# Kernel tuning notes

Hardware: AMD Instinct MI355X
Metric: run time of the kernel (lower is better)

## Reference

```python
import jax, jax.numpy as jnp
import numpy as np

N_NODES = 50000
N_EDGES = 500000
IN_DIM = 64
OUT_DIM = 64
NUM_RELS = 16


def setup_inputs() -> dict:
    key = jax.random.key(0)
    ks = jax.random.split(key, 8)
    h = jax.random.normal(ks[0], (N_NODES, IN_DIM), dtype=jnp.float32)
    he = jax.random.normal(ks[1], (N_EDGES, IN_DIM), dtype=jnp.float32)
    src = jax.random.randint(ks[2], (N_EDGES,), 0, N_NODES)
    dst = jax.random.randint(ks[3], (N_EDGES,), 0, N_NODES)
    rel = jax.random.randint(ks[4], (N_EDGES,), 0, NUM_RELS)
    # xavier-ish scales
    W_shared = jax.random.normal(ks[5], (OUT_DIM, IN_DIM), dtype=jnp.float32) * (2.0 / (IN_DIM + OUT_DIM)) ** 0.5
    W_attn = jax.random.normal(ks[6], (1, 3 * OUT_DIM), dtype=jnp.float32) * (2.0 / (3 * OUT_DIM + 1)) ** 0.5
    W_rel = jax.random.normal(ks[7], (NUM_RELS, IN_DIM, OUT_DIM), dtype=jnp.float32) * (2.0 / (IN_DIM + OUT_DIM)) ** 0.5
    return {"h": h, "he": he, "src": src, "dst": dst, "rel": rel,
            "W_shared": W_shared, "W_attn": W_attn, "W_rel": W_rel}


def reference(h, he, src, dst, rel, W_shared, W_attn, W_rel):
    # --- edge attention: a = attn_fc([z_src, z_edge, z_dst]) (raw linear score, no softmax in original) ---
    Z = h @ W_shared.T                      # [N, out] project all nodes once
    ze = he @ W_shared.T                    # [E, out]
    # split attn weight to avoid materializing [E, 3*out] concat
    Wa_s, Wa_e, Wa_d = jnp.split(W_attn, 3, axis=1)   # each [1, out]
    a = Z[src] @ Wa_s.T + ze @ Wa_e.T + Z[dst] @ Wa_d.T   # [E, 1]
    # --- message: msg = (h_src @ W_rel[rel]) * a ---
    # compute per-(node, relation) transform once [N, R, out], then gather per edge
    H_all = jnp.einsum('ni,rio->nro', h, W_rel)          # [N, R, out]
    msg = H_all[src, rel] * a                             # [E, out]
    # --- scatter-sum aggregation into destination nodes ---
    out = jax.ops.segment_sum(msg, dst, num_segments=N_NODES)  # [N, out]
    # apply_func: activation (relu), no bias
    return jax.nn.relu(out)
```

## Files before the change

kernel.cpp:

```cpp
#include <hip/hip_runtime.h>
#include <math.h>

#define N_NODES 50000
#define N_EDGES 500000
#define NUM_RELS 16
#define G3 64

typedef _Float16 f16x8 __attribute__((ext_vector_type(8)));
typedef float    f32x4 __attribute__((ext_vector_type(4)));


__global__ void kz(int* counts, int* cursor) {
    if (threadIdx.x < NUM_RELS) { counts[threadIdx.x] = 0; cursor[threadIdx.x] = 0; }
}

__global__ __launch_bounds__(256) void k_node(
    const float* __restrict__ h,
    const float* __restrict__ W_shared, const float* __restrict__ W_attn,
    const int* __restrict__ rel,
    float* __restrict__ sn, float* __restrict__ dn,
    float4* __restrict__ out4, int* __restrict__ counts) {
    __shared__ float sus[64], sud[64];
    __shared__ int hist[NUM_RELS];
    const int t = threadIdx.x, bid = blockIdx.x, nb = gridDim.x;
    if (t < 64) {
        float us = 0.f, ud = 0.f;
        for (int o = 0; o < 64; ++o) {
            float w = W_shared[o * 64 + t];
            us = fmaf(w, W_attn[o],       us);
            ud = fmaf(w, W_attn[128 + o], ud);
        }
        sus[t] = us; sud[t] = ud;
    }
    if (t < NUM_RELS) hist[t] = 0;
    __syncthreads();

    int n = bid * 256 + t;
    if (n < N_NODES) {
        const float* hp = h + (size_t)n * 64;
        float s = 0.f, d = 0.f;
#pragma unroll
        for (int i = 0; i < 64; i += 4) {
            float4 v = *(const float4*)(hp + i);
            s = fmaf(v.x, sus[i], s);     s = fmaf(v.y, sus[i + 1], s);
            s = fmaf(v.z, sus[i + 2], s); s = fmaf(v.w, sus[i + 3], s);
            d = fmaf(v.x, sud[i], d);     d = fmaf(v.y, sud[i + 1], d);
            d = fmaf(v.z, sud[i + 2], d); d = fmaf(v.w, sud[i + 3], d);
        }
        sn[n] = s; dn[n] = d;
        float4 z = make_float4(0.f, 0.f, 0.f, 0.f);
#pragma unroll
        for (int i = 0; i < 16; ++i) out4[(size_t)n * 16 + i] = z;
    }
    for (int e = bid * 256 + t; e < N_EDGES; e += nb * 256)
        atomicAdd(&hist[rel[e]], 1);
    __syncthreads();
    if (t < NUM_RELS && hist[t]) atomicAdd(&counts[t], hist[t]);
}

__global__ __launch_bounds__(256) void k_ae(
    const float4* __restrict__ he4,
    const int* __restrict__ src, const int* __restrict__ dst,
    const int* __restrict__ rel,
    const float* __restrict__ W_shared, const float* __restrict__ W_attn,
    const float* __restrict__ sn, const float* __restrict__ dn,
    const int* __restrict__ counts, int* __restrict__ cursor,
    int* __restrict__ srcs, int* __restrict__ dsts, float* __restrict__ aes) {
    __shared__ float sve[64];
    __shared__ int hist[NUM_RELS], bbase[NUM_RELS], soffs[NUM_RELS];
    const int t = threadIdx.x, bid = blockIdx.x, nb = gridDim.x;
    if (t < 64) {
        float ve = 0.f;
        for (int o = 0; o < 64; ++o)
            ve = fmaf(W_shared[o * 64 + t], W_attn[64 + o], ve);
        sve[t] = ve;
    }
    if (t == 0) {
        int acc = 0;
        for (int j = 0; j < NUM_RELS; ++j) { soffs[j] = acc; acc += counts[j]; }
    }
    for (int e0 = bid * 256; e0 < N_EDGES; e0 += nb * 256) {
        __syncthreads();
        if (t < NUM_RELS) hist[t] = 0;
        __syncthreads();
        int e = e0 + t;
        bool valid = (e < N_EDGES);
        int r = 0, lpos = 0, s_ = 0, d_ = 0; float aev = 0.f;
        if (valid) {
            s_ = src[e]; d_ = dst[e]; r = rel[e];
            const float4* hr = he4 + (size_t)e * 16;
            float acc = 0.f;
#pragma unroll
            for (int i = 0; i < 16; ++i) {
                float4 v = hr[i];
                float4 u = *(const float4*)(sve + 4 * i);
                acc += v.x * u.x + v.y * u.y + v.z * u.z + v.w * u.w;
            }
            aev = acc + sn[s_] + dn[d_];
            lpos = atomicAdd(&hist[r], 1);
        }
        __syncthreads();
        if (t < NUM_RELS) bbase[t] = hist[t] ? atomicAdd(&cursor[t], hist[t]) : 0;
        __syncthreads();
        if (valid) {
            int p = soffs[r] + bbase[r] + lpos;
            srcs[p] = s_; dsts[p] = d_; aes[p] = aev;
        }
    }
}

__global__ __launch_bounds__(256, 4) void k_mfma(
    const float* __restrict__ h, const float* __restrict__ W_rel,
    const int* __restrict__ counts,
    const int* __restrict__ srcs, const int* __restrict__ dsts,
    const float* __restrict__ aes, float* __restrict__ out)
{
    const int t = threadIdx.x;
    const int lane = t & 63;
    const int quad = lane >> 4;
    const int col  = lane & 15;
    const int wib  = t >> 6;
    const int r    = blockIdx.x & 15;
    const int g    = blockIdx.x >> 4;
    const int wr   = g * 4 + wib;
    const int WPR  = G3 * 4;

    int begin = 0, cr = 0;
#pragma unroll
    for (int j = 0; j < NUM_RELS; ++j) {
        int c = counts[j];
        if (j < r) begin += c;
        if (j == r) cr = c;
    }
    begin = __builtin_amdgcn_readfirstlane(begin);
    const int end = __builtin_amdgcn_readfirstlane(begin + cr);

    const float* Wb = W_rel + (size_t)r * 4096;

    for (int half = 0; half < 2; ++half) {
        f16x8 bh[2][2], bl[2][2];
#pragma unroll
        for (int kb = 0; kb < 2; ++kb)
#pragma unroll
            for (int n2 = 0; n2 < 2; ++n2)
#pragma unroll
                for (int j = 0; j < 8; ++j) {
                    float w = Wb[(kb * 32 + quad * 8 + j) * 64 + (half * 2 + n2) * 16 + col];
                    _Float16 hi = (_Float16)w;
                    bh[kb][n2][j] = hi;
                    bl[kb][n2][j] = (_Float16)(w - (float)hi);
                }

        for (int base = begin + wr * 16; base < end; base += WPR * 16) {
            int m16 = end - base; if (m16 > 16) m16 = 16;
            const int ridx = base + (col < m16 ? col : m16 - 1);
            const int   sv = srcs[ridx];
            const int   dv = dsts[ridx];
            const float av = (col < m16) ? aes[ridx] : 0.f;

            f16x8 ah[2], al[2];
            const float* hp = h + (size_t)sv * 64 + quad * 8;
#pragma unroll
            for (int kb = 0; kb < 2; ++kb) {
                float4 x = *(const float4*)(hp + kb * 32);
                float4 y = *(const float4*)(hp + kb * 32 + 4);
                float xs[8] = {x.x, x.y, x.z, x.w, y.x, y.y, y.z, y.w};
#pragma unroll
                for (int j = 0; j < 8; ++j) {
                    _Float16 hi = (_Float16)xs[j];
                    ah[kb][j] = hi;
                    al[kb][j] = (_Float16)(xs[j] - (float)hi);
                }
            }

            f32x4 acc0 = {0.f, 0.f, 0.f, 0.f};
            f32x4 acc1 = {0.f, 0.f, 0.f, 0.f};
#pragma unroll
            for (int kb = 0; kb < 2; ++kb) {
                acc0 = __builtin_amdgcn_mfma_f32_16x16x32_f16(ah[kb], bh[kb][0], acc0, 0, 0, 0);
                acc0 = __builtin_amdgcn_mfma_f32_16x16x32_f16(ah[kb], bl[kb][0], acc0, 0, 0, 0);
                acc0 = __builtin_amdgcn_mfma_f32_16x16x32_f16(al[kb], bh[kb][0], acc0, 0, 0, 0);
                acc1 = __builtin_amdgcn_mfma_f32_16x16x32_f16(ah[kb], bh[kb][1], acc1, 0, 0, 0);
                acc1 = __builtin_amdgcn_mfma_f32_16x16x32_f16(ah[kb], bl[kb][1], acc1, 0, 0, 0);
                acc1 = __builtin_amdgcn_mfma_f32_16x16x32_f16(al[kb], bh[kb][1], acc1, 0, 0, 0);
            }

#pragma unroll
            for (int reg = 0; reg < 4; ++reg) {
                const int m = quad * 4 + reg;
                const int   dm = __shfl(dv, m, 64);
                const float am = __shfl(av, m, 64);
                float* op = out + (size_t)dm * 64 + half * 32 + col;
                unsafeAtomicAdd(op,      am * acc0[reg]);
                unsafeAtomicAdd(op + 16, am * acc1[reg]);
            }
        }
    }
}

__global__ __launch_bounds__(256) void k_relu(float4* __restrict__ out4) {
    for (int i = blockIdx.x * 256 + threadIdx.x; i < N_NODES * 16; i += gridDim.x * 256) {
        float4 v = out4[i];
        v.x = fmaxf(v.x, 0.f); v.y = fmaxf(v.y, 0.f);
        v.z = fmaxf(v.z, 0.f); v.w = fmaxf(v.w, 0.f);
        out4[i] = v;
    }
}

extern "C" void kernel_launch(void* const* d_in, const int* in_sizes, int n_in,
                              void* d_out, int out_size, void* d_ws, size_t ws_size,
                              hipStream_t stream) {
    const float*  h        = (const float*)d_in[0];
    const float4* he4      = (const float4*)d_in[1];
    const int*    src      = (const int*)d_in[2];
    const int*    dst      = (const int*)d_in[3];
    const int*    rel      = (const int*)d_in[4];
    const float*  W_shared = (const float*)d_in[5];
    const float*  W_attn   = (const float*)d_in[6];
    const float*  W_rel    = (const float*)d_in[7];
    float*        out      = (float*)d_out;

    int*   counts = (int*)d_ws + 192;
    int*   cursor = (int*)d_ws + 228;
    float* sn     = (float*)d_ws + 256;
    float* dn     = (float*)d_ws + 50256;
    int*   srcs   = (int*)d_ws + 100352;
    int*   dsts   = (int*)d_ws + 600352;
    float* aes    = (float*)d_ws + 1100352;

    kz<<<1, 64, 0, stream>>>(counts, cursor);
    k_node<<<(N_NODES + 255) / 256, 256, 0, stream>>>(h, W_shared, W_attn, rel,
                                                      sn, dn, (float4*)out, counts);
    k_ae<<<1024, 256, 0, stream>>>(he4, src, dst, rel, W_shared, W_attn,
                                   sn, dn, counts, cursor, srcs, dsts, aes);
    k_mfma<<<NUM_RELS * G3, 256, 0, stream>>>(h, W_rel, counts, srcs, dsts, aes, out);
    k_relu<<<1024, 256, 0, stream>>>((float4*)out);
}
```

Measured before the change: 350.9 us.

## Precompute fp16 hi/lo split of h, split halves across blocks, prefetch gathers

```diff
diff --git a/kernel.cpp b/kernel.cpp
--- a/kernel.cpp
+++ b/kernel.cpp
@@ -4,9 +4,10 @@
 #define N_NODES 50000
 #define N_EDGES 500000
 #define NUM_RELS 16
-#define G3 64
+#define GH 64
 
 typedef _Float16 f16x8 __attribute__((ext_vector_type(8)));
+typedef _Float16 f16x4 __attribute__((ext_vector_type(4)));
 typedef float    f32x4 __attribute__((ext_vector_type(4)));
 
 
@@ -19,7 +20,8 @@
     const float* __restrict__ W_shared, const float* __restrict__ W_attn,
     const int* __restrict__ rel,
     float* __restrict__ sn, float* __restrict__ dn,
-    float4* __restrict__ out4, int* __restrict__ counts) {
+    float4* __restrict__ out4, int* __restrict__ counts,
+    _Float16* __restrict__ h_hi, _Float16* __restrict__ h_lo) {
     __shared__ float sus[64], sud[64];
     __shared__ int hist[NUM_RELS];
     const int t = threadIdx.x, bid = blockIdx.x, nb = gridDim.x;
@@ -46,6 +48,13 @@
             s = fmaf(v.z, sus[i + 2], s); s = fmaf(v.w, sus[i + 3], s);
             d = fmaf(v.x, sud[i], d);     d = fmaf(v.y, sud[i + 1], d);
             d = fmaf(v.z, sud[i + 2], d); d = fmaf(v.w, sud[i + 3], d);
+            f16x4 hi, lo;
+            hi[0] = (_Float16)v.x; lo[0] = (_Float16)(v.x - (float)hi[0]);
+            hi[1] = (_Float16)v.y; lo[1] = (_Float16)(v.y - (float)hi[1]);
+            hi[2] = (_Float16)v.z; lo[2] = (_Float16)(v.z - (float)hi[2]);
+            hi[3] = (_Float16)v.w; lo[3] = (_Float16)(v.w - (float)hi[3]);
+            *(f16x4*)(h_hi + (size_t)n * 64 + i) = hi;
+            *(f16x4*)(h_lo + (size_t)n * 64 + i) = lo;
         }
         sn[n] = s; dn[n] = d;
         float4 z = make_float4(0.f, 0.f, 0.f, 0.f);
@@ -110,7 +119,8 @@
 }
 
 __global__ __launch_bounds__(256, 4) void k_mfma(
-    const float* __restrict__ h, const float* __restrict__ W_rel,
+    const _Float16* __restrict__ h_hi, const _Float16* __restrict__ h_lo,
+    const float* __restrict__ W_rel,
     const int* __restrict__ counts,
     const int* __restrict__ srcs, const int* __restrict__ dsts,
     const float* __restrict__ aes, float* __restrict__ out)
@@ -120,10 +130,13 @@
     const int quad = lane >> 4;
     const int col  = lane & 15;
     const int wib  = t >> 6;
-    const int r    = blockIdx.x & 15;
-    const int g    = blockIdx.x >> 4;
+    const int rh   = blockIdx.x & 31;
+    const int r    = rh & 15;
+    const int half = rh >> 4;
+    const int g    = blockIdx.x >> 5;
     const int wr   = g * 4 + wib;
-    const int WPR  = G3 * 4;
+    const int WPR  = GH * 4;
+    const int STEP = WPR * 16;
 
     int begin = 0, cr = 0;
 #pragma unroll
@@ -136,65 +149,79 @@
     const int end = __builtin_amdgcn_readfirstlane(begin + cr);
 
     const float* Wb = W_rel + (size_t)r * 4096;
-
-    for (int half = 0; half < 2; ++half) {
-        f16x8 bh[2][2], bl[2][2];
-#pragma unroll
-        for (int kb = 0; kb < 2; ++kb)
-#pragma unroll
-            for (int n2 = 0; n2 < 2; ++n2)
-#pragma unroll
-                for (int j = 0; j < 8; ++j) {
-                    float w = Wb[(kb * 32 + quad * 8 + j) * 64 + (half * 2 + n2) * 16 + col];
-                    _Float16 hi = (_Float16)w;
-                    bh[kb][n2][j] = hi;
-                    bl[kb][n2][j] = (_Float16)(w - (float)hi);
-                }
-
-        for (int base = begin + wr * 16; base < end; base += WPR * 16) {
-            int m16 = end - base; if (m16 > 16) m16 = 16;
-            const int ridx = base + (col < m16 ? col : m16 - 1);
-            const int   sv = srcs[ridx];
-            const int   dv = dsts[ridx];
-            const float av = (col < m16) ? aes[ridx] : 0.f;
-
-            f16x8 ah[2], al[2];
-            const float* hp = h + (size_t)sv * 64 + quad * 8;
-#pragma unroll
-            for (int kb = 0; kb < 2; ++kb) {
-                float4 x = *(const float4*)(hp + kb * 32);
-                float4 y = *(const float4*)(hp + kb * 32 + 4);
-                float xs[8] = {x.x, x.y, x.z, x.w, y.x, y.y, y.z, y.w};
-#pragma unroll
-                for (int j = 0; j < 8; ++j) {
-                    _Float16 hi = (_Float16)xs[j];
-                    ah[kb][j] = hi;
-                    al[kb][j] = (_Float16)(xs[j] - (float)hi);
-                }
+    f16x8 bh[2][2], bl[2][2];
+#pragma unroll
+    for (int kb = 0; kb < 2; ++kb)
+#pragma unroll
+        for (int n2 = 0; n2 < 2; ++n2)
+#pragma unroll
+            for (int j = 0; j < 8; ++j) {
+                float w = Wb[(kb * 32 + quad * 8 + j) * 64 + (half * 2 + n2) * 16 + col];
+                _Float16 hi = (_Float16)w;
+                bh[kb][n2][j] = hi;
+                bl[kb][n2][j] = (_Float16)(w - (float)hi);
             }
 
-            f32x4 acc0 = {0.f, 0.f, 0.f, 0.f};
-            f32x4 acc1 = {0.f, 0.f, 0.f, 0.f};
-#pragma unroll
-            for (int kb = 0; kb < 2; ++kb) {
-                acc0 = __builtin_amdgcn_mfma_f32_16x16x32_f16(ah[kb], bh[kb][0], acc0, 0, 0, 0);
-                acc0 = __builtin_amdgcn_mfma_f32_16x16x32_f16(ah[kb], bl[kb][0], acc0, 0, 0, 0);
-                acc0 = __builtin_amdgcn_mfma_f32_16x16x32_f16(al[kb], bh[kb][0], acc0, 0, 0, 0);
-                acc1 = __builtin_amdgcn_mfma_f32_16x16x32_f16(ah[kb], bh[kb][1], acc1, 0, 0, 0);
-                acc1 = __builtin_amdgcn_mfma_f32_16x16x32_f16(ah[kb], bl[kb][1], acc1, 0, 0, 0);
-                acc1 = __builtin_amdgcn_mfma_f32_16x16x32_f16(al[kb], bh[kb][1], acc1, 0, 0, 0);
-            }
-
-#pragma unroll
-            for (int reg = 0; reg < 4; ++reg) {
-                const int m = quad * 4 + reg;
-                const int   dm = __shfl(dv, m, 64);
-                const float am = __shfl(av, m, 64);
-                float* op = out + (size_t)dm * 64 + half * 32 + col;
-                unsafeAtomicAdd(op,      am * acc0[reg]);
-                unsafeAtomicAdd(op + 16, am * acc1[reg]);
-            }
-        }
+    int base = begin + wr * 16;
+    if (base >= end) return;
+
+    int sv0, dv0; float av0;
+    {
+        int m16 = end - base; if (m16 > 16) m16 = 16;
+        int ridx = base + (col < m16 ? col : m16 - 1);
+        sv0 = srcs[ridx]; dv0 = dsts[ridx];
+        av0 = (col < m16) ? aes[ridx] : 0.f;
+    }
+    f16x8 ah0, ah1, al0, al1;
+    {
+        const _Float16* ph = h_hi + (size_t)sv0 * 64 + quad * 8;
+        const _Float16* pl = h_lo + (size_t)sv0 * 64 + quad * 8;
+        ah0 = *(const f16x8*)ph;        ah1 = *(const f16x8*)(ph + 32);
+        al0 = *(const f16x8*)pl;        al1 = *(const f16x8*)(pl + 32);
+    }
+
+    for (; base < end; base += STEP) {
+        const int nb = base + STEP;
+        int sv1 = 0, dv1 = 0; float av1 = 0.f;
+        f16x8 nah0, nah1, nal0, nal1;
+        if (nb < end) {
+            int m16 = end - nb; if (m16 > 16) m16 = 16;
+            int ridx = nb + (col < m16 ? col : m16 - 1);
+            sv1 = srcs[ridx]; dv1 = dsts[ridx];
+            av1 = (col < m16) ? aes[ridx] : 0.f;
+            const _Float16* ph = h_hi + (size_t)sv1 * 64 + quad * 8;
+            const _Float16* pl = h_lo + (size_t)sv1 * 64 + quad * 8;
+            nah0 = *(const f16x8*)ph;   nah1 = *(const f16x8*)(ph + 32);
+            nal0 = *(const f16x8*)pl;   nal1 = *(const f16x8*)(pl + 32);
+        }
+
+        f32x4 acc0 = {0.f, 0.f, 0.f, 0.f};
+        f32x4 acc1 = {0.f, 0.f, 0.f, 0.f};
+        acc0 = __builtin_amdgcn_mfma_f32_16x16x32_f16(ah0, bh[0][0], acc0, 0, 0, 0);
+        acc1 = __builtin_amdgcn_mfma_f32_16x16x32_f16(ah0, bh[0][1], acc1, 0, 0, 0);
+        acc0 = __builtin_amdgcn_mfma_f32_16x16x32_f16(ah0, bl[0][0], acc0, 0, 0, 0);
+        acc1 = __builtin_amdgcn_mfma_f32_16x16x32_f16(ah0, bl[0][1], acc1, 0, 0, 0);
+        acc0 = __builtin_amdgcn_mfma_f32_16x16x32_f16(al0, bh[0][0], acc0, 0, 0, 0);
+        acc1 = __builtin_amdgcn_mfma_f32_16x16x32_f16(al0, bh[0][1], acc1, 0, 0, 0);
+        acc0 = __builtin_amdgcn_mfma_f32_16x16x32_f16(ah1, bh[1][0], acc0, 0, 0, 0);
+        acc1 = __builtin_amdgcn_mfma_f32_16x16x32_f16(ah1, bh[1][1], acc1, 0, 0, 0);
+        acc0 = __builtin_amdgcn_mfma_f32_16x16x32_f16(ah1, bl[1][0], acc0, 0, 0, 0);
+        acc1 = __builtin_amdgcn_mfma_f32_16x16x32_f16(ah1, bl[1][1], acc1, 0, 0, 0);
+        acc0 = __builtin_amdgcn_mfma_f32_16x16x32_f16(al1, bh[1][0], acc0, 0, 0, 0);
+        acc1 = __builtin_amdgcn_mfma_f32_16x16x32_f16(al1, bh[1][1], acc1, 0, 0, 0);
+
+#pragma unroll
+        for (int reg = 0; reg < 4; ++reg) {
+            const int m = quad * 4 + reg;
+            const int   dm = __shfl(dv0, m, 64);
+            const float am = __shfl(av0, m, 64);
+            float* op = out + (size_t)dm * 64 + half * 32 + col;
+            unsafeAtomicAdd(op,      am * acc0[reg]);
+            unsafeAtomicAdd(op + 16, am * acc1[reg]);
+        }
+
+        sv0 = sv1; dv0 = dv1; av0 = av1;
+        ah0 = nah0; ah1 = nah1; al0 = nal0; al1 = nal1;
     }
 }
 
@@ -220,19 +247,22 @@
     const float*  W_rel    = (const float*)d_in[7];
     float*        out      = (float*)d_out;
 
-    int*   counts = (int*)d_ws + 192;
-    int*   cursor = (int*)d_ws + 228;
-    float* sn     = (float*)d_ws + 256;
-    float* dn     = (float*)d_ws + 50256;
-    int*   srcs   = (int*)d_ws + 100352;
-    int*   dsts   = (int*)d_ws + 600352;
-    float* aes    = (float*)d_ws + 1100352;
+    int*      counts = (int*)d_ws + 192;
+    int*      cursor = (int*)d_ws + 228;
+    float*    sn     = (float*)d_ws + 256;
+    float*    dn     = (float*)d_ws + 50256;
+    int*      srcs   = (int*)d_ws + 100352;
+    int*      dsts   = (int*)d_ws + 600352;
+    float*    aes    = (float*)d_ws + 1100352;
+    _Float16* h_hi   = (_Float16*)((int*)d_ws + 1600352);
+    _Float16* h_lo   = (_Float16*)((int*)d_ws + 3200352);
 
     kz<<<1, 64, 0, stream>>>(counts, cursor);
     k_node<<<(N_NODES + 255) / 256, 256, 0, stream>>>(h, W_shared, W_attn, rel,
-                                                      sn, dn, (float4*)out, counts);
-    k_ae<<<1024, 256, 0, stream>>>(he4, src, dst, rel, W_shared, W_attn,
+                                                      sn, dn, (float4*)out, counts,
+                                                      h_hi, h_lo);
+    k_ae<<<2048, 256, 0, stream>>>(he4, src, dst, rel, W_shared, W_attn,
                                    sn, dn, counts, cursor, srcs, dsts, aes);
-    k_mfma<<<NUM_RELS * G3, 256, 0, stream>>>(h, W_rel, counts, srcs, dsts, aes, out);
+    k_mfma<<<32 * GH, 256, 0, stream>>>(h_hi, h_lo, W_rel, counts, srcs, dsts, aes, out);
     k_relu<<<1024, 256, 0, stream>>>((float4*)out);
 }
```

After: 358.6 us. +2.2%, slower.

## Bucket edges by destination block and relation, aggregate in shared memory

Applied to the files above, without the earlier changes.

```diff
diff --git a/kernel.cpp b/kernel.cpp
--- a/kernel.cpp
+++ b/kernel.cpp
@@ -4,24 +4,28 @@
 #define N_NODES 50000
 #define N_EDGES 500000
 #define NUM_RELS 16
-#define G3 64
+#define DSTB 64
+#define NBLK_AGG 782
+#define NKEY (NBLK_AGG * NUM_RELS)
 
 typedef _Float16 f16x8 __attribute__((ext_vector_type(8)));
+typedef _Float16 f16x4 __attribute__((ext_vector_type(4)));
 typedef float    f32x4 __attribute__((ext_vector_type(4)));
 
 
-__global__ void kz(int* counts, int* cursor) {
-    if (threadIdx.x < NUM_RELS) { counts[threadIdx.x] = 0; cursor[threadIdx.x] = 0; }
+__global__ void kz(int* __restrict__ counts, int* __restrict__ cursor) {
+    int i = blockIdx.x * 256 + threadIdx.x;
+    if (i < NKEY) { counts[i] = 0; cursor[i] = 0; }
 }
 
 __global__ __launch_bounds__(256) void k_node(
     const float* __restrict__ h,
     const float* __restrict__ W_shared, const float* __restrict__ W_attn,
-    const int* __restrict__ rel,
+    const int* __restrict__ dst, const int* __restrict__ rel,
     float* __restrict__ sn, float* __restrict__ dn,
-    float4* __restrict__ out4, int* __restrict__ counts) {
+    int* __restrict__ counts,
+    _Float16* __restrict__ h_hi, _Float16* __restrict__ h_lo) {
     __shared__ float sus[64], sud[64];
-    __shared__ int hist[NUM_RELS];
     const int t = threadIdx.x, bid = blockIdx.x, nb = gridDim.x;
     if (t < 64) {
         float us = 0.f, ud = 0.f;
@@ -32,7 +36,6 @@
         }
         sus[t] = us; sud[t] = ud;
     }
-    if (t < NUM_RELS) hist[t] = 0;
     __syncthreads();
 
     int n = bid * 256 + t;
@@ -46,16 +49,45 @@
             s = fmaf(v.z, sus[i + 2], s); s = fmaf(v.w, sus[i + 3], s);
             d = fmaf(v.x, sud[i], d);     d = fmaf(v.y, sud[i + 1], d);
             d = fmaf(v.z, sud[i + 2], d); d = fmaf(v.w, sud[i + 3], d);
+            f16x4 hi, lo;
+            hi[0] = (_Float16)v.x; lo[0] = (_Float16)(v.x - (float)hi[0]);
+            hi[1] = (_Float16)v.y; lo[1] = (_Float16)(v.y - (float)hi[1]);
+            hi[2] = (_Float16)v.z; lo[2] = (_Float16)(v.z - (float)hi[2]);
+            hi[3] = (_Float16)v.w; lo[3] = (_Float16)(v.w - (float)hi[3]);
+            *(f16x4*)(h_hi + (size_t)n * 64 + i) = hi;
+            *(f16x4*)(h_lo + (size_t)n * 64 + i) = lo;
         }
         sn[n] = s; dn[n] = d;
-        float4 z = make_float4(0.f, 0.f, 0.f, 0.f);
-#pragma unroll
-        for (int i = 0; i < 16; ++i) out4[(size_t)n * 16 + i] = z;
-    }
-    for (int e = bid * 256 + t; e < N_EDGES; e += nb * 256)
-        atomicAdd(&hist[rel[e]], 1);
-    __syncthreads();
-    if (t < NUM_RELS && hist[t]) atomicAdd(&counts[t], hist[t]);
+    }
+    for (int e = bid * 256 + t; e < N_EDGES; e += nb * 256) {
+        int key = (dst[e] >> 6) * NUM_RELS + rel[e];
+        atomicAdd(&counts[key], 1);
+    }
+}
+
+__global__ __launch_bounds__(1024) void k_scan(const int* __restrict__ counts,
+                                               int* __restrict__ offs) {
+    __shared__ int part[1024];
+    const int t = threadIdx.x;
+    const int C = 13;
+    int s = 0;
+    for (int j = 0; j < C; ++j) {
+        int idx = t * C + j;
+        if (idx < NKEY) s += counts[idx];
+    }
+    part[t] = s;
+    __syncthreads();
+    if (t == 0) {
+        int a = 0;
+        for (int i = 0; i < 1024; ++i) { int v = part[i]; part[i] = a; a += v; }
+    }
+    __syncthreads();
+    int a = part[t];
+    for (int j = 0; j < C; ++j) {
+        int idx = t * C + j;
+        if (idx < NKEY)       { offs[idx] = a; a += counts[idx]; }
+        else if (idx == NKEY) { offs[idx] = a; }
+    }
 }
 
 __global__ __launch_bounds__(256) void k_ae(
@@ -64,10 +96,9 @@
     const int* __restrict__ rel,
     const float* __restrict__ W_shared, const float* __restrict__ W_attn,
     const float* __restrict__ sn, const float* __restrict__ dn,
-    const int* __restrict__ counts, int* __restrict__ cursor,
+    const int* __restrict__ offs, int* __restrict__ cursor,
     int* __restrict__ srcs, int* __restrict__ dsts, float* __restrict__ aes) {
     __shared__ float sve[64];
-    __shared__ int hist[NUM_RELS], bbase[NUM_RELS], soffs[NUM_RELS];
     const int t = threadIdx.x, bid = blockIdx.x, nb = gridDim.x;
     if (t < 64) {
         float ve = 0.f;
@@ -75,135 +106,112 @@
             ve = fmaf(W_shared[o * 64 + t], W_attn[64 + o], ve);
         sve[t] = ve;
     }
-    if (t == 0) {
-        int acc = 0;
-        for (int j = 0; j < NUM_RELS; ++j) { soffs[j] = acc; acc += counts[j]; }
-    }
-    for (int e0 = bid * 256; e0 < N_EDGES; e0 += nb * 256) {
-        __syncthreads();
-        if (t < NUM_RELS) hist[t] = 0;
-        __syncthreads();
-        int e = e0 + t;
-        bool valid = (e < N_EDGES);
-        int r = 0, lpos = 0, s_ = 0, d_ = 0; float aev = 0.f;
-        if (valid) {
-            s_ = src[e]; d_ = dst[e]; r = rel[e];
-            const float4* hr = he4 + (size_t)e * 16;
-            float acc = 0.f;
-#pragma unroll
-            for (int i = 0; i < 16; ++i) {
-                float4 v = hr[i];
-                float4 u = *(const float4*)(sve + 4 * i);
-                acc += v.x * u.x + v.y * u.y + v.z * u.z + v.w * u.w;
-            }
-            aev = acc + sn[s_] + dn[d_];
-            lpos = atomicAdd(&hist[r], 1);
-        }
-        __syncthreads();
-        if (t < NUM_RELS) bbase[t] = hist[t] ? atomicAdd(&cursor[t], hist[t]) : 0;
-        __syncthreads();
-        if (valid) {
-            int p = soffs[r] + bbase[r] + lpos;
-            srcs[p] = s_; dsts[p] = d_; aes[p] = aev;
-        }
-    }
-}
-
-__global__ __launch_bounds__(256, 4) void k_mfma(
-    const float* __restrict__ h, const float* __restrict__ W_rel,
-    const int* __restrict__ counts,
+    __syncthreads();
+    for (int e = bid * 256 + t; e < N_EDGES; e += nb * 256) {
+        int s_ = src[e], d_ = dst[e], r_ = rel[e];
+        const float4* hr = he4 + (size_t)e * 16;
+        float acc = 0.f;
+#pragma unroll
+        for (int i = 0; i < 16; ++i) {
+            float4 v = hr[i];
+            float4 u = *(const float4*)(sve + 4 * i);
+            acc += v.x * u.x + v.y * u.y + v.z * u.z + v.w * u.w;
+        }
+        float aev = acc + sn[s_] + dn[d_];
+        int key = (d_ >> 6) * NUM_RELS + r_;
+        int pos = offs[key] + atomicAdd(&cursor[key], 1);
+        srcs[pos] = s_; dsts[pos] = d_; aes[pos] = aev;
+    }
+}
+
+__global__ __launch_bounds__(256, 4) void k_agg(
+    const _Float16* __restrict__ h_hi, const _Float16* __restrict__ h_lo,
+    const float* __restrict__ W_rel, const int* __restrict__ offs,
     const int* __restrict__ srcs, const int* __restrict__ dsts,
     const float* __restrict__ aes, float* __restrict__ out)
 {
-    const int t = threadIdx.x;
+    __shared__ float accum[DSTB * 68];
+    const int t = threadIdx.x, b = blockIdx.x;
     const int lane = t & 63;
+    const int wib  = t >> 6;
     const int quad = lane >> 4;
     const int col  = lane & 15;
-    const int wib  = t >> 6;
-    const int r    = blockIdx.x & 15;
-    const int g    = blockIdx.x >> 4;
-    const int wr   = g * 4 + wib;
-    const int WPR  = G3 * 4;
-
-    int begin = 0, cr = 0;
-#pragma unroll
-    for (int j = 0; j < NUM_RELS; ++j) {
-        int c = counts[j];
-        if (j < r) begin += c;
-        if (j == r) cr = c;
-    }
-    begin = __builtin_amdgcn_readfirstlane(begin);
-    const int end = __builtin_amdgcn_readfirstlane(begin + cr);
-
-    const float* Wb = W_rel + (size_t)r * 4096;
-
-    for (int half = 0; half < 2; ++half) {
-        f16x8 bh[2][2], bl[2][2];
+
+    for (int i = t; i < DSTB * 68; i += 256) accum[i] = 0.f;
+    __syncthreads();
+
+    for (int rr = 0; rr < 4; ++rr) {
+        const int r = wib + rr * 4;
+        const int segbeg = __builtin_amdgcn_readfirstlane(offs[b * NUM_RELS + r]);
+        const int segend = __builtin_amdgcn_readfirstlane(offs[b * NUM_RELS + r + 1]);
+        if (segbeg >= segend) continue;
+
+        const float* Wb = W_rel + (size_t)r * 4096;
+        f16x8 bh[2][4], bl[2][4];
 #pragma unroll
         for (int kb = 0; kb < 2; ++kb)
 #pragma unroll
-            for (int n2 = 0; n2 < 2; ++n2)
+            for (int nt = 0; nt < 4; ++nt)
 #pragma unroll
                 for (int j = 0; j < 8; ++j) {
-                    float w = Wb[(kb * 32 + quad * 8 + j) * 64 + (half * 2 + n2) * 16 + col];
+                    float w = Wb[(kb * 32 + quad * 8 + j) * 64 + nt * 16 + col];
                     _Float16 hi = (_Float16)w;
-                    bh[kb][n2][j] = hi;
-                    bl[kb][n2][j] = (_Float16)(w - (float)hi);
+                    bh[kb][nt][j] = hi;
+                    bl[kb][nt][j] = (_Float16)(w - (float)hi);
                 }
 
-        for (int base = begin + wr * 16; base < end; base += WPR * 16) {
-            int m16 = end - base; if (m16 > 16) m16 = 16;
+        for (int base = segbeg; base < segend; base += 16) {
+            int m16 = segend - base; if (m16 > 16) m16 = 16;
             const int ridx = base + (col < m16 ? col : m16 - 1);
             const int   sv = srcs[ridx];
             const int   dv = dsts[ridx];
             const float av = (col < m16) ? aes[ridx] : 0.f;
 
-            f16x8 ah[2], al[2];
-            const float* hp = h + (size_t)sv * 64 + quad * 8;
-#pragma unroll
-            for (int kb = 0; kb < 2; ++kb) {
-                float4 x = *(const float4*)(hp + kb * 32);
-                float4 y = *(const float4*)(hp + kb * 32 + 4);
-                float xs[8] = {x.x, x.y, x.z, x.w, y.x, y.y, y.z, y.w};
-#pragma unroll
-                for (int j = 0; j < 8; ++j) {
-                    _Float16 hi = (_Float16)xs[j];
-                    ah[kb][j] = hi;
-                    al[kb][j] = (_Float16)(xs[j] - (float)hi);
-                }
-            }
-
-            f32x4 acc0 = {0.f, 0.f, 0.f, 0.f};
-            f32x4 acc1 = {0.f, 0.f, 0.f, 0.f};
-#pragma unroll
-            for (int kb = 0; kb < 2; ++kb) {
-                acc0 = __builtin_amdgcn_mfma_f32_16x16x32_f16(ah[kb], bh[kb][0], acc0, 0, 0, 0);
-                acc0 = __builtin_amdgcn_mfma_f32_16x16x32_f16(ah[kb], bl[kb][0], acc0, 0, 0, 0);
-                acc0 = __builtin_amdgcn_mfma_f32_16x16x32_f16(al[kb], bh[kb][0], acc0, 0, 0, 0);
-                acc1 = __builtin_amdgcn_mfma_f32_16x16x32_f16(ah[kb], bh[kb][1], acc1, 0, 0, 0);
-                acc1 = __builtin_amdgcn_mfma_f32_16x16x32_f16(ah[kb], bl[kb][1], acc1, 0, 0, 0);
-                acc1 = __builtin_amdgcn_mfma_f32_16x16x32_f16(al[kb], bh[kb][1], acc1, 0, 0, 0);
+            const _Float16* ph = h_hi + (size_t)sv * 64 + quad * 8;
+            const _Float16* pl = h_lo + (size_t)sv * 64 + quad * 8;
+            f16x8 ah0 = *(const f16x8*)ph,        ah1 = *(const f16x8*)(ph + 32);
+            f16x8 al0 = *(const f16x8*)pl,        al1 = *(const f16x8*)(pl + 32);
+
+            f32x4 acc[4];
+#pragma unroll
+            for (int nt = 0; nt < 4; ++nt) acc[nt] = (f32x4){0.f, 0.f, 0.f, 0.f};
+#pragma unroll
+            for (int nt = 0; nt < 4; ++nt) {
+                acc[nt] = __builtin_amdgcn_mfma_f32_16x16x32_f16(ah0, bh[0][nt], acc[nt], 0, 0, 0);
+                acc[nt] = __builtin_amdgcn_mfma_f32_16x16x32_f16(ah0, bl[0][nt], acc[nt], 0, 0, 0);
+                acc[nt] = __builtin_amdgcn_mfma_f32_16x16x32_f16(al0, bh[0][nt], acc[nt], 0, 0, 0);
+                acc[nt] = __builtin_amdgcn_mfma_f32_16x16x32_f16(ah1, bh[1][nt], acc[nt], 0, 0, 0);
+                acc[nt] = __builtin_amdgcn_mfma_f32_16x16x32_f16(ah1, bl[1][nt], acc[nt], 0, 0, 0);
+                acc[nt] = __builtin_amdgcn_mfma_f32_16x16x32_f16(al1, bh[1][nt], acc[nt], 0, 0, 0);
             }
 
 #pragma unroll
             for (int reg = 0; reg < 4; ++reg) {
                 const int m = quad * 4 + reg;
-                const int   dm = __shfl(dv, m, 64);
+                const int   dm = __shfl(dv, m, 64) & (DSTB - 1);
                 const float am = __shfl(av, m, 64);
-                float* op = out + (size_t)dm * 64 + half * 32 + col;
-                unsafeAtomicAdd(op,      am * acc0[reg]);
-                unsafeAtomicAdd(op + 16, am * acc1[reg]);
+                float* ap = accum + dm * 68 + col;
+#pragma unroll
+                for (int nt = 0; nt < 4; ++nt)
+                    atomicAdd(ap + nt * 16, am * acc[nt][reg]);
             }
         }
     }
-}
-
-__global__ __launch_bounds__(256) void k_relu(float4* __restrict__ out4) {
-    for (int i = blockIdx.x * 256 + threadIdx.x; i < N_NODES * 16; i += gridDim.x * 256) {
-        float4 v = out4[i];
-        v.x = fmaxf(v.x, 0.f); v.y = fmaxf(v.y, 0.f);
-        v.z = fmaxf(v.z, 0.f); v.w = fmaxf(v.w, 0.f);
-        out4[i] = v;
+    __syncthreads();
+
+    const int i  = t >> 2;
+    const int c0 = (t & 3) * 16;
+    const int node = b * DSTB + i;
+    if (node < N_NODES) {
+        float* op = out + (size_t)node * 64 + c0;
+        const float* ap = accum + i * 68 + c0;
+#pragma unroll
+        for (int k = 0; k < 4; ++k) {
+            float4 v = *(const float4*)(ap + 4 * k);
+            v.x = fmaxf(v.x, 0.f); v.y = fmaxf(v.y, 0.f);
+            v.z = fmaxf(v.z, 0.f); v.w = fmaxf(v.w, 0.f);
+            *(float4*)(op + 4 * k) = v;
+        }
     }
 }
 
@@ -220,19 +228,23 @@
     const float*  W_rel    = (const float*)d_in[7];
     float*        out      = (float*)d_out;
 
-    int*   counts = (int*)d_ws + 192;
-    int*   cursor = (int*)d_ws + 228;
-    float* sn     = (float*)d_ws + 256;
-    float* dn     = (float*)d_ws + 50256;
-    int*   srcs   = (int*)d_ws + 100352;
-    int*   dsts   = (int*)d_ws + 600352;
-    float* aes    = (float*)d_ws + 1100352;
-
-    kz<<<1, 64, 0, stream>>>(counts, cursor);
-    k_node<<<(N_NODES + 255) / 256, 256, 0, stream>>>(h, W_shared, W_attn, rel,
-                                                      sn, dn, (float4*)out, counts);
-    k_ae<<<1024, 256, 0, stream>>>(he4, src, dst, rel, W_shared, W_attn,
-                                   sn, dn, counts, cursor, srcs, dsts, aes);
-    k_mfma<<<NUM_RELS * G3, 256, 0, stream>>>(h, W_rel, counts, srcs, dsts, aes, out);
-    k_relu<<<1024, 256, 0, stream>>>((float4*)out);
-}
+    int*      counts = (int*)d_ws + 0;
+    int*      cursor = (int*)d_ws + 12544;
+    int*      offs   = (int*)d_ws + 25088;
+    float*    sn     = (float*)d_ws + 37632;
+    float*    dn     = (float*)d_ws + 87632;
+    int*      srcs   = (int*)d_ws + 137632;
+    int*      dsts   = (int*)d_ws + 637632;
+    float*    aes    = (float*)d_ws + 1137632;
+    _Float16* h_hi   = (_Float16*)((int*)d_ws + 1637632);
+    _Float16* h_lo   = (_Float16*)((int*)d_ws + 3237632);
+
+    kz<<<(NKEY + 255) / 256, 256, 0, stream>>>(counts, cursor);
+    k_node<<<392, 256, 0, stream>>>(h, W_shared, W_attn, dst, rel,
+                                    sn, dn, counts, h_hi, h_lo);
+    k_scan<<<1, 1024, 0, stream>>>(counts, offs);
+    k_ae<<<2048, 256, 0, stream>>>(he4, src, dst, rel, W_shared, W_attn,
+                                   sn, dn, offs, cursor, srcs, dsts, aes);
+    k_agg<<<NBLK_AGG, 256, 0, stream>>>(h_hi, h_lo, W_rel, offs,
+                                        srcs, dsts, aes, out);
+}
```

Measured after the change: 581.2 us. 65.7% more time.
